# Kernel tuning notes

Measured on AMD Instinct MI355X. Metric: run time of the kernel, lower is better.

## Reference

```python
import jax, jax.numpy as jnp
import numpy as np

B, S, D, H = 1, 512, 128, 128
EPS = 1e-5


def layernorm(x, g, b):
    mu = jnp.mean(x, axis=-1, keepdims=True)
    var = jnp.mean(jnp.square(x - mu), axis=-1, keepdims=True)
    return (x - mu) * jax.lax.rsqrt(var + EPS) * g + b


def setup_inputs() -> dict:
    key = jax.random.key(0)
    ks = jax.random.split(key, 10)
    scale_d = 1.0 / np.sqrt(D)
    scale_h = 1.0 / np.sqrt(H)
    return {
        "x": jax.random.normal(ks[0], (B, S, S, D), dtype=jnp.float32),
        "mask": jax.random.uniform(ks[1], (B, S, S), dtype=jnp.float32),
        "norm_g": jnp.ones((D,), jnp.float32),
        "norm_b": jnp.zeros((D,), jnp.float32),
        "Wl": jax.random.normal(ks[2], (H, D), jnp.float32) * scale_d,
        "Wr": jax.random.normal(ks[3], (H, D), jnp.float32) * scale_d,
        "Wlg": jax.random.normal(ks[4], (H, D), jnp.float32) * scale_d,
        "Wrg": jax.random.normal(ks[5], (H, D), jnp.float32) * scale_d,
        "Wog": jax.random.normal(ks[6], (H, D), jnp.float32) * scale_d,
        "out_norm_g": jnp.ones((H,), jnp.float32),
        "out_norm_b": jnp.zeros((H,), jnp.float32),
        "Wout": jax.random.normal(ks[7], (D, H), jnp.float32) * scale_h,
    }


def reference(x, mask, norm_g, norm_b, Wl, Wr, Wlg, Wrg, Wog, out_norm_g, out_norm_b, Wout):
    # x: [B,S,S,D], mask: [B,S,S]
    xn = layernorm(x, norm_g, norm_b)
    m = mask[..., None]  # [B,S,S,1]
    left = (xn @ Wl.T) * m * jax.nn.sigmoid(xn @ Wlg.T)   # [B,S,S,H]
    right = (xn @ Wr.T) * m * jax.nn.sigmoid(xn @ Wrg.T)  # [B,S,S,H]
    out_gate = jax.nn.sigmoid(xn @ Wog.T)                  # [B,S,S,H]
    # per-channel triangular contraction over k
    out = jnp.einsum('bikd,bjkd->bijd', left, right)       # [B,S,S,H]
    out = layernorm(out, out_norm_g, out_norm_b) * out_gate
    return out @ Wout.T  # [B,S,S,D]
```

## Files before the change

### kernel.cpp

```cpp
#include <hip/hip_runtime.h>
#include <hip/hip_bf16.h>
#include <cstdint>

typedef unsigned short u16;
typedef unsigned int   u32;
typedef __bf16 bf16x8 __attribute__((ext_vector_type(8)));
typedef float  f32x4  __attribute__((ext_vector_type(4)));

#define S_    512
#define D_    128
#define H_    128
#define NPOS_ (S_ * S_)
#define LN_EPS 1e-5f

__device__ __forceinline__ u16 f2bf(float f) {
  union { __hip_bfloat16 h; u16 u; } cv;
  cv.h = __float2bfloat16(f);
  return cv.u;
}
__device__ __forceinline__ float bflo(u32 p) { return __uint_as_float(p << 16); }
__device__ __forceinline__ float bfhi(u32 p) { return __uint_as_float(p & 0xffff0000u); }
__device__ __forceinline__ float sigmoidf_(float x) { return 1.f / (1.f + __expf(-x)); }

__device__ __forceinline__ void gld16(const void* g, void* l) {
  __builtin_amdgcn_global_load_lds(
      (const __attribute__((address_space(1))) void*)g,
      (__attribute__((address_space(3))) void*)l, 16, 0, 0);
}

template <int CPR, int TOTAL>
__device__ __forceinline__ void stage_tile(const char* gbase, int ld_bytes, char* lds, int tid) {
#pragma unroll
  for (int c = tid; c < TOTAL; c += 256) {
    int row = c / CPR;
    int col = c - row * CPR;
    gld16(gbase + (size_t)row * ld_bytes + (size_t)col * 16, lds + (size_t)c * 16);
  }
}

__global__ __launch_bounds__(256) void k_prep(
    const float* __restrict__ wl, const float* __restrict__ wlg,
    const float* __restrict__ wr, const float* __restrict__ wrg,
    const float* __restrict__ wog, const float* __restrict__ wout,
    u16* __restrict__ wb) {
  int i = blockIdx.x * 256 + threadIdx.x;
  int m = i >> 14, o = i & 16383;
  const float* src = (m == 0) ? wl : (m == 1) ? wlg : (m == 2) ? wr
                   : (m == 3) ? wrg : (m == 4) ? wog : wout;
  wb[i] = f2bf(src[o]);
}

__global__ __launch_bounds__(256) void k_ln(
    const float* __restrict__ x, const float* __restrict__ ng,
    const float* __restrict__ nb, u32* __restrict__ xn) {
  const int l  = threadIdx.x & 63;
  const int wid = (blockIdx.x * 256 + threadIdx.x) >> 6;
  const int nw  = (gridDim.x * 256) >> 6;
  const float2 gg = ((const float2*)ng)[l];
  const float2 bb = ((const float2*)nb)[l];
  for (int row = wid; row < NPOS_; row += nw) {
    float2 v = ((const float2*)(x + (size_t)row * D_))[l];
    float s = v.x + v.y;
    float q = v.x * v.x + v.y * v.y;
#pragma unroll
    for (int off = 32; off >= 1; off >>= 1) {
      s += __shfl_xor(s, off);
      q += __shfl_xor(q, off);
    }
    float mu  = s * (1.f / 128.f);
    float var = q * (1.f / 128.f) - mu * mu;
    float rs  = rsqrtf(var + LN_EPS);
    float a = (v.x - mu) * rs * gg.x + bb.x;
    float b = (v.y - mu) * rs * gg.y + bb.y;
    xn[(size_t)row * 64 + l] = (u32)f2bf(a) | ((u32)f2bf(b) << 16);
  }
}

__global__ __launch_bounds__(256, 2) void k_proj(
    const u16* __restrict__ xn, const float* __restrict__ mask,
    const u16* __restrict__ wb, u16* __restrict__ left_t,
    u16* __restrict__ right_t, u16* __restrict__ gate_t) {
  __shared__ u16 Bs[128 * 64];
  __shared__ u16 As0[128 * 64];
  __shared__ u16 As1[128 * 64];
  const int g   = blockIdx.y;
  const int r0  = blockIdx.x * 128;
  const int tid = threadIdx.x;
  const int w = tid >> 6, l = tid & 63;
  const int wr = w >> 1, wc = w & 1;
  const u16* W0 = wb + (size_t)((g == 2) ? 4 : 2 * g) * (H_ * D_);
  const u16* W1 = wb + (size_t)(2 * g + 1) * (H_ * D_);

  const f32x4 vz = {0.f, 0.f, 0.f, 0.f};
  f32x4 acc0[4][4], acc1[4][4];
#pragma unroll
  for (int i = 0; i < 4; ++i)
#pragma unroll
    for (int j = 0; j < 4; ++j) { acc0[i][j] = vz; acc1[i][j] = vz; }

#pragma unroll
  for (int kt = 0; kt < 2; ++kt) {
    stage_tile<8, 1024>((const char*)xn + ((size_t)r0 * D_ + kt * 64) * 2, D_ * 2, (char*)Bs, tid);
    stage_tile<8, 1024>((const char*)W0 + (size_t)(kt * 64) * 2, D_ * 2, (char*)As0, tid);
    if (g < 2)
      stage_tile<8, 1024>((const char*)W1 + (size_t)(kt * 64) * 2, D_ * 2, (char*)As1, tid);
    __syncthreads();
#pragma unroll
    for (int kk = 0; kk < 2; ++kk) {
      const int ko = kk * 32 + (l >> 4) * 8;
      bf16x8 bfr[4], a0[4], a1[4];
#pragma unroll
      for (int ni = 0; ni < 4; ++ni)
        bfr[ni] = *(const bf16x8*)&Bs[(wc * 64 + ni * 16 + (l & 15)) * 64 + ko];
#pragma unroll
      for (int mi = 0; mi < 4; ++mi)
        a0[mi] = *(const bf16x8*)&As0[(wr * 64 + mi * 16 + (l & 15)) * 64 + ko];
      if (g < 2) {
#pragma unroll
        for (int mi = 0; mi < 4; ++mi)
          a1[mi] = *(const bf16x8*)&As1[(wr * 64 + mi * 16 + (l & 15)) * 64 + ko];
      }
#pragma unroll
      for (int mi = 0; mi < 4; ++mi)
#pragma unroll
        for (int ni = 0; ni < 4; ++ni) {
          acc0[mi][ni] = __builtin_amdgcn_mfma_f32_16x16x32_bf16(a0[mi], bfr[ni], acc0[mi][ni], 0, 0, 0);
          if (g < 2)
            acc1[mi][ni] = __builtin_amdgcn_mfma_f32_16x16x32_bf16(a1[mi], bfr[ni], acc1[mi][ni], 0, 0, 0);
        }
    }
    __syncthreads();
  }

  const int quad = l >> 4, lc = l & 15;
  u16* dst = (g == 0) ? left_t : (g == 1) ? right_t : gate_t;
#pragma unroll
  for (int ni = 0; ni < 4; ++ni) {
    const int r = r0 + wc * 64 + ni * 16 + lc;
    const float mk = (g < 2) ? mask[r] : 0.f;
#pragma unroll
    for (int mi = 0; mi < 4; ++mi) {
#pragma unroll
      for (int reg = 0; reg < 4; ++reg) {
        const int hrow = wr * 64 + mi * 16 + quad * 4 + reg;
        float v0 = acc0[mi][ni][reg];
        float o;
        if (g < 2) o = v0 * mk * sigmoidf_(acc1[mi][ni][reg]);
        else       o = sigmoidf_(v0);
        dst[(size_t)hrow * NPOS_ + r] = f2bf(o);
      }
    }
  }
}

__global__ __launch_bounds__(256, 2) void k_einsum(
    const u16* __restrict__ left_t, const u16* __restrict__ right_t,
    u16* __restrict__ out_t) {
  const int d = blockIdx.x;
  const int t = blockIdx.y;
  const int i0 = (t >> 2) * 128, j0 = (t & 3) * 128;
  __shared__ u16 As[128 * 64], Bs[128 * 64];
  const u16* L = left_t + (size_t)d * NPOS_;
  const u16* R = right_t + (size_t)d * NPOS_;
  const int tid = threadIdx.x;
  const int w = tid >> 6, l = tid & 63;
  const int wr = w >> 1, wc = w & 1;

  const f32x4 vz = {0.f, 0.f, 0.f, 0.f};
  f32x4 acc[4][4];
#pragma unroll
  for (int i = 0; i < 4; ++i)
#pragma unroll
    for (int j = 0; j < 4; ++j) acc[i][j] = vz;

  for (int kt = 0; kt < 8; ++kt) {
    stage_tile<8, 1024>((const char*)L + ((size_t)i0 * S_ + kt * 64) * 2, S_ * 2, (char*)As, tid);
    stage_tile<8, 1024>((const char*)R + ((size_t)j0 * S_ + kt * 64) * 2, S_ * 2, (char*)Bs, tid);
    __syncthreads();
#pragma unroll
    for (int kk = 0; kk < 2; ++kk) {
      const int ko = kk * 32 + (l >> 4) * 8;
      bf16x8 a[4], b[4];
#pragma unroll
      for (int mi = 0; mi < 4; ++mi)
        a[mi] = *(const bf16x8*)&As[(wr * 64 + mi * 16 + (l & 15)) * 64 + ko];
#pragma unroll
      for (int ni = 0; ni < 4; ++ni)
        b[ni] = *(const bf16x8*)&Bs[(wc * 64 + ni * 16 + (l & 15)) * 64 + ko];
#pragma unroll
      for (int mi = 0; mi < 4; ++mi)
#pragma unroll
        for (int ni = 0; ni < 4; ++ni)
          acc[mi][ni] = __builtin_amdgcn_mfma_f32_16x16x32_bf16(a[mi], b[ni], acc[mi][ni], 0, 0, 0);
    }
    __syncthreads();
  }

  const int quad = l >> 4, lc = l & 15;
  u16* O = out_t + (size_t)d * NPOS_;
#pragma unroll
  for (int mi = 0; mi < 4; ++mi)
#pragma unroll
    for (int ni = 0; ni < 4; ++ni) {
      const int col = j0 + wc * 64 + ni * 16 + lc;
#pragma unroll
      for (int reg = 0; reg < 4; ++reg) {
        const int row = i0 + wr * 64 + mi * 16 + quad * 4 + reg;
        O[(size_t)row * S_ + col] = f2bf(acc[mi][ni][reg]);
      }
    }
}

__global__ __launch_bounds__(256, 2) void k_final(
    const u16* __restrict__ out_t, const u16* __restrict__ gate_t,
    const float* __restrict__ og, const float* __restrict__ ob,
    const u16* __restrict__ wout_b, float* __restrict__ out) {
  __shared__ u16 A_lds[128 * 136];
  __shared__ u16 Wlds[128 * 128];
  __shared__ float psum[4][128], pq[4][128];
  __shared__ float mu_s[128], rs_s[128];
  const int tid = threadIdx.x, w = tid >> 6, l = tid & 63;
  const int r0 = blockIdx.x * 128;

  stage_tile<16, 2048>((const char*)wout_b, 256, (char*)Wlds, tid);

  float s0 = 0.f, s1 = 0.f, q0 = 0.f, q1 = 0.f;
  for (int it = 0; it < 32; ++it) {
    int d = it * 4 + w;
    u32 p = *(const u32*)&out_t[(size_t)d * NPOS_ + r0 + 2 * l];
    float f0 = bflo(p), f1 = bfhi(p);
    s0 += f0; s1 += f1; q0 += f0 * f0; q1 += f1 * f1;
  }
  psum[w][2 * l] = s0; psum[w][2 * l + 1] = s1;
  pq[w][2 * l] = q0;   pq[w][2 * l + 1] = q1;
  __syncthreads();
  if (tid < 128) {
    float s = psum[0][tid] + psum[1][tid] + psum[2][tid] + psum[3][tid];
    float q = pq[0][tid] + pq[1][tid] + pq[2][tid] + pq[3][tid];
    float mu  = s * (1.f / 128.f);
    float var = q * (1.f / 128.f) - mu * mu;
    mu_s[tid] = mu;
    rs_s[tid] = rsqrtf(var + LN_EPS);
  }
  __syncthreads();

  for (int it = 0; it < 32; ++it) {
    int d = it * 4 + w;
    u32 p  = *(const u32*)&out_t[(size_t)d * NPOS_ + r0 + 2 * l];
    u32 gp = *(const u32*)&gate_t[(size_t)d * NPOS_ + r0 + 2 * l];
    float gd = og[d], bd = ob[d];
    float f0 = bflo(p), f1 = bfhi(p);
    float g0 = bflo(gp), g1 = bfhi(gp);
    int ja = 2 * l, jb = 2 * l + 1;
    float a0 = ((f0 - mu_s[ja]) * rs_s[ja] * gd + bd) * g0;
    float a1 = ((f1 - mu_s[jb]) * rs_s[jb] * gd + bd) * g1;
    A_lds[(size_t)ja * 136 + d] = f2bf(a0);
    A_lds[(size_t)jb * 136 + d] = f2bf(a1);
  }
  __syncthreads();

  const int wr = w >> 1, wc = w & 1;
  const f32x4 vz = {0.f, 0.f, 0.f, 0.f};
  f32x4 acc[4][4];
#pragma unroll
  for (int i = 0; i < 4; ++i)
#pragma unroll
    for (int j = 0; j < 4; ++j) acc[i][j] = vz;
#pragma unroll
  for (int kk = 0; kk < 4; ++kk) {
    const int ko = kk * 32 + (l >> 4) * 8;
    bf16x8 a[4], b[4];
#pragma unroll
    for (int mi = 0; mi < 4; ++mi)
      a[mi] = *(const bf16x8*)&A_lds[(wr * 64 + mi * 16 + (l & 15)) * 136 + ko];
#pragma unroll
    for (int ni = 0; ni < 4; ++ni)
      b[ni] = *(const bf16x8*)&Wlds[(wc * 64 + ni * 16 + (l & 15)) * 128 + ko];
#pragma unroll
    for (int mi = 0; mi < 4; ++mi)
#pragma unroll
      for (int ni = 0; ni < 4; ++ni)
        acc[mi][ni] = __builtin_amdgcn_mfma_f32_16x16x32_bf16(a[mi], b[ni], acc[mi][ni], 0, 0, 0);
  }
  const int quad = l >> 4, lc = l & 15;
#pragma unroll
  for (int mi = 0; mi < 4; ++mi)
#pragma unroll
    for (int ni = 0; ni < 4; ++ni) {
      const int dout = wc * 64 + ni * 16 + lc;
#pragma unroll
      for (int reg = 0; reg < 4; ++reg) {
        const int row = r0 + wr * 64 + mi * 16 + quad * 4 + reg;
        out[(size_t)row * D_ + dout] = acc[mi][ni][reg];
      }
    }
}

extern "C" void kernel_launch(void* const* d_in, const int* in_sizes, int n_in,
                              void* d_out, int out_size, void* d_ws, size_t ws_size,
                              hipStream_t stream) {
  const float* x    = (const float*)d_in[0];
  const float* mask = (const float*)d_in[1];
  const float* ng   = (const float*)d_in[2];
  const float* nb   = (const float*)d_in[3];
  const float* Wl   = (const float*)d_in[4];
  const float* Wr   = (const float*)d_in[5];
  const float* Wlg  = (const float*)d_in[6];
  const float* Wrg  = (const float*)d_in[7];
  const float* Wog  = (const float*)d_in[8];
  const float* og   = (const float*)d_in[9];
  const float* ob   = (const float*)d_in[10];
  const float* Wout = (const float*)d_in[11];
  float* out = (float*)d_out;

  const size_t SLAB = (size_t)NPOS_ * H_ * 2;
  char* ws = (char*)d_ws;
  u16* xn      = (u16*)(ws);
  u16* left_t  = (u16*)(ws + SLAB);
  u16* right_t = (u16*)(ws + 2 * SLAB);
  u16* gate_t  = (u16*)(ws + 3 * SLAB);
  u16* wb      = (u16*)(ws + 4 * SLAB);
  u16* out_t   = xn;
  if (ws_size < 4 * SLAB + 6 * H_ * D_ * sizeof(u16)) return;

  k_prep<<<384, 256, 0, stream>>>(Wl, Wlg, Wr, Wrg, Wog, Wout, wb);
  k_ln<<<2048, 256, 0, stream>>>(x, ng, nb, (u32*)xn);
  k_proj<<<dim3(2048, 3), 256, 0, stream>>>(xn, mask, wb, left_t, right_t, gate_t);
  k_einsum<<<dim3(128, 16), 256, 0, stream>>>(left_t, right_t, out_t);
  k_final<<<2048, 256, 0, stream>>>(out_t, gate_t, og, ob, wb + 5 * H_ * D_, out);
}
```

Baseline: 495.1 us.

## Swizzle LDS tiles, split projection into pair and gate kernels, raise occupancy

Adds an XOR swizzle to every global-to-LDS staging path and fragment read to remove LDS bank conflicts in the MFMA GEMMs. The projection kernel is split into a 512-thread pair kernel, where value and gate waves each own one accumulator set and exchange sigmoids through LDS, and a separate gate-only kernel, so no block carries a second unused accumulator set. Launch bounds are raised to 4 blocks per CU. The bf16 conversion is replaced by manual round-to-nearest-even bit math and sigmoid uses a hardware reciprocal. This adds an extra LDS round trip and barrier in the pair kernel and one more kernel launch.

```diff
diff --git a/kernel.cpp b/kernel.cpp
--- a/kernel.cpp
+++ b/kernel.cpp
@@ -14,13 +14,21 @@
 #define LN_EPS 1e-5f
 
 __device__ __forceinline__ u16 f2bf(float f) {
-  union { __hip_bfloat16 h; u16 u; } cv;
-  cv.h = __float2bfloat16(f);
-  return cv.u;
+  u32 u = __float_as_uint(f);
+  u += 0x7fff + ((u >> 16) & 1);
+  return (u16)(u >> 16);
+}
+__device__ __forceinline__ u32 f2bf2(float lo, float hi) {
+  u32 a = __float_as_uint(lo); a += 0x7fff + ((a >> 16) & 1);
+  u32 b = __float_as_uint(hi); b += 0x7fff + ((b >> 16) & 1);
+  return (a >> 16) | (b & 0xffff0000u);
 }
 __device__ __forceinline__ float bflo(u32 p) { return __uint_as_float(p << 16); }
 __device__ __forceinline__ float bfhi(u32 p) { return __uint_as_float(p & 0xffff0000u); }
-__device__ __forceinline__ float sigmoidf_(float x) { return 1.f / (1.f + __expf(-x)); }
+__device__ __forceinline__ float bf2f(u16 v) { return __uint_as_float((u32)v << 16); }
+__device__ __forceinline__ float sigmoidf_(float x) {
+  return __builtin_amdgcn_rcpf(1.f + __expf(-x));
+}
 
 __device__ __forceinline__ void gld16(const void* g, void* l) {
   __builtin_amdgcn_global_load_lds(
@@ -28,14 +36,23 @@
       (__attribute__((address_space(3))) void*)l, 16, 0, 0);
 }
 
-template <int CPR, int TOTAL>
-__device__ __forceinline__ void stage_tile(const char* gbase, int ld_bytes, char* lds, int tid) {
-#pragma unroll
-  for (int c = tid; c < TOTAL; c += 256) {
-    int row = c / CPR;
-    int col = c - row * CPR;
-    gld16(gbase + (size_t)row * ld_bytes + (size_t)col * 16, lds + (size_t)c * 16);
-  }
+template <int CPR, int TOTAL, int THREADS>
+__device__ __forceinline__ void stage_sw(const char* gbase, int ld_bytes, char* lds, int tid) {
+#pragma unroll
+  for (int c = tid; c < TOTAL; c += THREADS) {
+    int row  = c / CPR;
+    int colL = c & (CPR - 1);
+    int colG = colL ^ (row & (CPR - 1));
+    gld16(gbase + (size_t)row * ld_bytes + (size_t)colG * 16, lds + (size_t)c * 16);
+  }
+}
+__device__ __forceinline__ bf16x8 frag8(const u16* lds, int row, int ko) {
+  int chunk = (ko >> 3) ^ (row & 7);
+  return *(const bf16x8*)&lds[row * 64 + (chunk << 3)];
+}
+__device__ __forceinline__ bf16x8 frag16(const u16* lds, int row, int ko) {
+  int chunk = (ko >> 3) ^ (row & 15);
+  return *(const bf16x8*)&lds[row * 128 + (chunk << 3)];
 }
 
 __global__ __launch_bounds__(256) void k_prep(
@@ -72,88 +89,147 @@
     float rs  = rsqrtf(var + LN_EPS);
     float a = (v.x - mu) * rs * gg.x + bb.x;
     float b = (v.y - mu) * rs * gg.y + bb.y;
-    xn[(size_t)row * 64 + l] = (u32)f2bf(a) | ((u32)f2bf(b) << 16);
-  }
-}
-
-__global__ __launch_bounds__(256, 2) void k_proj(
+    xn[(size_t)row * 64 + l] = f2bf2(a, b);
+  }
+}
+
+__global__ __launch_bounds__(512, 4) void k_proj_pair(
     const u16* __restrict__ xn, const float* __restrict__ mask,
     const u16* __restrict__ wb, u16* __restrict__ left_t,
-    u16* __restrict__ right_t, u16* __restrict__ gate_t) {
+    u16* __restrict__ right_t) {
   __shared__ u16 Bs[128 * 64];
-  __shared__ u16 As0[128 * 64];
-  __shared__ u16 As1[128 * 64];
+  __shared__ u16 As[2 * 128 * 64];
   const int g   = blockIdx.y;
   const int r0  = blockIdx.x * 128;
   const int tid = threadIdx.x;
   const int w = tid >> 6, l = tid & 63;
-  const int wr = w >> 1, wc = w & 1;
-  const u16* W0 = wb + (size_t)((g == 2) ? 4 : 2 * g) * (H_ * D_);
-  const u16* W1 = wb + (size_t)(2 * g + 1) * (H_ * D_);
+  const int role = w >> 2, sub = w & 3;
+  const int wr = sub >> 1, wc = sub & 1;
+  const u16* Wv = wb + (size_t)(2 * g) * (H_ * D_);
+  const u16* Wg = Wv + H_ * D_;
+  const u16* Amine = As + role * (128 * 64);
 
   const f32x4 vz = {0.f, 0.f, 0.f, 0.f};
-  f32x4 acc0[4][4], acc1[4][4];
+  f32x4 acc[4][4];
 #pragma unroll
   for (int i = 0; i < 4; ++i)
 #pragma unroll
-    for (int j = 0; j < 4; ++j) { acc0[i][j] = vz; acc1[i][j] = vz; }
+    for (int j = 0; j < 4; ++j) acc[i][j] = vz;
 
 #pragma unroll
   for (int kt = 0; kt < 2; ++kt) {
-    stage_tile<8, 1024>((const char*)xn + ((size_t)r0 * D_ + kt * 64) * 2, D_ * 2, (char*)Bs, tid);
-    stage_tile<8, 1024>((const char*)W0 + (size_t)(kt * 64) * 2, D_ * 2, (char*)As0, tid);
-    if (g < 2)
-      stage_tile<8, 1024>((const char*)W1 + (size_t)(kt * 64) * 2, D_ * 2, (char*)As1, tid);
+    stage_sw<8, 1024, 512>((const char*)xn + ((size_t)r0 * D_ + kt * 64) * 2, D_ * 2, (char*)Bs, tid);
+    stage_sw<8, 1024, 512>((const char*)Wv + (size_t)(kt * 64) * 2, D_ * 2, (char*)As, tid);
+    stage_sw<8, 1024, 512>((const char*)Wg + (size_t)(kt * 64) * 2, D_ * 2, (char*)(As + 128 * 64), tid);
     __syncthreads();
 #pragma unroll
     for (int kk = 0; kk < 2; ++kk) {
       const int ko = kk * 32 + (l >> 4) * 8;
-      bf16x8 bfr[4], a0[4], a1[4];
-#pragma unroll
-      for (int ni = 0; ni < 4; ++ni)
-        bfr[ni] = *(const bf16x8*)&Bs[(wc * 64 + ni * 16 + (l & 15)) * 64 + ko];
-#pragma unroll
-      for (int mi = 0; mi < 4; ++mi)
-        a0[mi] = *(const bf16x8*)&As0[(wr * 64 + mi * 16 + (l & 15)) * 64 + ko];
-      if (g < 2) {
-#pragma unroll
-        for (int mi = 0; mi < 4; ++mi)
-          a1[mi] = *(const bf16x8*)&As1[(wr * 64 + mi * 16 + (l & 15)) * 64 + ko];
+      bf16x8 bfr[4];
+#pragma unroll
+      for (int ni = 0; ni < 4; ++ni)
+        bfr[ni] = frag8(Bs, wc * 64 + ni * 16 + (l & 15), ko);
+#pragma unroll
+      for (int mi = 0; mi < 4; ++mi) {
+        bf16x8 a = frag8(Amine, wr * 64 + mi * 16 + (l & 15), ko);
+#pragma unroll
+        for (int ni = 0; ni < 4; ++ni)
+          acc[mi][ni] = __builtin_amdgcn_mfma_f32_16x16x32_bf16(a, bfr[ni], acc[mi][ni], 0, 0, 0);
       }
-#pragma unroll
-      for (int mi = 0; mi < 4; ++mi)
-#pragma unroll
-        for (int ni = 0; ni < 4; ++ni) {
-          acc0[mi][ni] = __builtin_amdgcn_mfma_f32_16x16x32_bf16(a0[mi], bfr[ni], acc0[mi][ni], 0, 0, 0);
-          if (g < 2)
-            acc1[mi][ni] = __builtin_amdgcn_mfma_f32_16x16x32_bf16(a1[mi], bfr[ni], acc1[mi][ni], 0, 0, 0);
+    }
+    __syncthreads();
+  }
+
+  const int quad = l >> 4, lc = l & 15;
+  u16* G = As;
+  if (role == 1) {
+#pragma unroll
+    for (int mi = 0; mi < 4; ++mi)
+#pragma unroll
+      for (int ni = 0; ni < 4; ++ni)
+#pragma unroll
+        for (int reg = 0; reg < 4; ++reg) {
+          int idx = (mi * 4 + ni) * 4 + reg;
+          G[(sub * 64 + idx) * 64 + l] = f2bf(sigmoidf_(acc[mi][ni][reg]));
         }
+  }
+  __syncthreads();
+  if (role == 0) {
+    u16* dst = (g == 0) ? left_t : right_t;
+    float mk[4];
+#pragma unroll
+    for (int ni = 0; ni < 4; ++ni) mk[ni] = mask[r0 + wc * 64 + ni * 16 + lc];
+#pragma unroll
+    for (int mi = 0; mi < 4; ++mi)
+#pragma unroll
+      for (int ni = 0; ni < 4; ++ni)
+#pragma unroll
+        for (int reg = 0; reg < 4; ++reg) {
+          int idx = (mi * 4 + ni) * 4 + reg;
+          float sg = bf2f(G[(sub * 64 + idx) * 64 + l]);
+          int r = r0 + wc * 64 + ni * 16 + lc;
+          int hrow = wr * 64 + mi * 16 + quad * 4 + reg;
+          dst[(size_t)hrow * NPOS_ + r] = f2bf(acc[mi][ni][reg] * mk[ni] * sg);
+        }
+  }
+}
+
+__global__ __launch_bounds__(256, 4) void k_proj_gate(
+    const u16* __restrict__ xn, const u16* __restrict__ wb,
+    u16* __restrict__ gate_t) {
+  __shared__ u16 Bs[128 * 64];
+  __shared__ u16 As0[128 * 64];
+  const int r0  = blockIdx.x * 128;
+  const int tid = threadIdx.x;
+  const int w = tid >> 6, l = tid & 63;
+  const int wr = w >> 1, wc = w & 1;
+  const u16* W0 = wb + (size_t)4 * (H_ * D_);
+
+  const f32x4 vz = {0.f, 0.f, 0.f, 0.f};
+  f32x4 acc[4][4];
+#pragma unroll
+  for (int i = 0; i < 4; ++i)
+#pragma unroll
+    for (int j = 0; j < 4; ++j) acc[i][j] = vz;
+
+#pragma unroll
+  for (int kt = 0; kt < 2; ++kt) {
+    stage_sw<8, 1024, 256>((const char*)xn + ((size_t)r0 * D_ + kt * 64) * 2, D_ * 2, (char*)Bs, tid);
+    stage_sw<8, 1024, 256>((const char*)W0 + (size_t)(kt * 64) * 2, D_ * 2, (char*)As0, tid);
+    __syncthreads();
+#pragma unroll
+    for (int kk = 0; kk < 2; ++kk) {
+      const int ko = kk * 32 + (l >> 4) * 8;
+      bf16x8 bfr[4];
+#pragma unroll
+      for (int ni = 0; ni < 4; ++ni)
+        bfr[ni] = frag8(Bs, wc * 64 + ni * 16 + (l & 15), ko);
+#pragma unroll
+      for (int mi = 0; mi < 4; ++mi) {
+        bf16x8 a = frag8(As0, wr * 64 + mi * 16 + (l & 15), ko);
+#pragma unroll
+        for (int ni = 0; ni < 4; ++ni)
+          acc[mi][ni] = __builtin_amdgcn_mfma_f32_16x16x32_bf16(a, bfr[ni], acc[mi][ni], 0, 0, 0);
+      }
     }
     __syncthreads();
   }
 
   const int quad = l >> 4, lc = l & 15;
-  u16* dst = (g == 0) ? left_t : (g == 1) ? right_t : gate_t;
 #pragma unroll
   for (int ni = 0; ni < 4; ++ni) {
     const int r = r0 + wc * 64 + ni * 16 + lc;
-    const float mk = (g < 2) ? mask[r] : 0.f;
-#pragma unroll
-    for (int mi = 0; mi < 4; ++mi) {
+#pragma unroll
+    for (int mi = 0; mi < 4; ++mi)
 #pragma unroll
       for (int reg = 0; reg < 4; ++reg) {
         const int hrow = wr * 64 + mi * 16 + quad * 4 + reg;
-        float v0 = acc0[mi][ni][reg];
-        float o;
-        if (g < 2) o = v0 * mk * sigmoidf_(acc1[mi][ni][reg]);
-        else       o = sigmoidf_(v0);
-        dst[(size_t)hrow * NPOS_ + r] = f2bf(o);
+        gate_t[(size_t)hrow * NPOS_ + r] = f2bf(sigmoidf_(acc[mi][ni][reg]));
       }
-    }
-  }
-}
-
-__global__ __launch_bounds__(256, 2) void k_einsum(
+  }
+}
+
+__global__ __launch_bounds__(256, 4) void k_einsum(
     const u16* __restrict__ left_t, const u16* __restrict__ right_t,
     u16* __restrict__ out_t) {
   const int d = blockIdx.x;
@@ -174,8 +250,8 @@
     for (int j = 0; j < 4; ++j) acc[i][j] = vz;
 
   for (int kt = 0; kt < 8; ++kt) {
-    stage_tile<8, 1024>((const char*)L + ((size_t)i0 * S_ + kt * 64) * 2, S_ * 2, (char*)As, tid);
-    stage_tile<8, 1024>((const char*)R + ((size_t)j0 * S_ + kt * 64) * 2, S_ * 2, (char*)Bs, tid);
+    stage_sw<8, 1024, 256>((const char*)L + ((size_t)i0 * S_ + kt * 64) * 2, S_ * 2, (char*)As, tid);
+    stage_sw<8, 1024, 256>((const char*)R + ((size_t)j0 * S_ + kt * 64) * 2, S_ * 2, (char*)Bs, tid);
     __syncthreads();
 #pragma unroll
     for (int kk = 0; kk < 2; ++kk) {
@@ -183,10 +259,10 @@
       bf16x8 a[4], b[4];
 #pragma unroll
       for (int mi = 0; mi < 4; ++mi)
-        a[mi] = *(const bf16x8*)&As[(wr * 64 + mi * 16 + (l & 15)) * 64 + ko];
-#pragma unroll
-      for (int ni = 0; ni < 4; ++ni)
-        b[ni] = *(const bf16x8*)&Bs[(wc * 64 + ni * 16 + (l & 15)) * 64 + ko];
+        a[mi] = frag8(As, wr * 64 + mi * 16 + (l & 15), ko);
+#pragma unroll
+      for (int ni = 0; ni < 4; ++ni)
+        b[ni] = frag8(Bs, wc * 64 + ni * 16 + (l & 15), ko);
 #pragma unroll
       for (int mi = 0; mi < 4; ++mi)
 #pragma unroll
@@ -222,7 +298,7 @@
   const int tid = threadIdx.x, w = tid >> 6, l = tid & 63;
   const int r0 = blockIdx.x * 128;
 
-  stage_tile<16, 2048>((const char*)wout_b, 256, (char*)Wlds, tid);
+  stage_sw<16, 2048, 256>((const char*)wout_b, 256, (char*)Wlds, tid);
 
   float s0 = 0.f, s1 = 0.f, q0 = 0.f, q1 = 0.f;
   for (int it = 0; it < 32; ++it) {
@@ -252,10 +328,8 @@
     float f0 = bflo(p), f1 = bfhi(p);
     float g0 = bflo(gp), g1 = bfhi(gp);
     int ja = 2 * l, jb = 2 * l + 1;
-    float a0 = ((f0 - mu_s[ja]) * rs_s[ja] * gd + bd) * g0;
-    float a1 = ((f1 - mu_s[jb]) * rs_s[jb] * gd + bd) * g1;
-    A_lds[(size_t)ja * 136 + d] = f2bf(a0);
-    A_lds[(size_t)jb * 136 + d] = f2bf(a1);
+    A_lds[(size_t)ja * 136 + d] = f2bf(((f0 - mu_s[ja]) * rs_s[ja] * gd + bd) * g0);
+    A_lds[(size_t)jb * 136 + d] = f2bf(((f1 - mu_s[jb]) * rs_s[jb] * gd + bd) * g1);
   }
   __syncthreads();
 
@@ -275,7 +349,7 @@
       a[mi] = *(const bf16x8*)&A_lds[(wr * 64 + mi * 16 + (l & 15)) * 136 + ko];
 #pragma unroll
     for (int ni = 0; ni < 4; ++ni)
-      b[ni] = *(const bf16x8*)&Wlds[(wc * 64 + ni * 16 + (l & 15)) * 128 + ko];
+      b[ni] = frag16(Wlds, wc * 64 + ni * 16 + (l & 15), ko);
 #pragma unroll
     for (int mi = 0; mi < 4; ++mi)
 #pragma unroll
@@ -325,7 +399,8 @@
 
   k_prep<<<384, 256, 0, stream>>>(Wl, Wlg, Wr, Wrg, Wog, Wout, wb);
   k_ln<<<2048, 256, 0, stream>>>(x, ng, nb, (u32*)xn);
-  k_proj<<<dim3(2048, 3), 256, 0, stream>>>(xn, mask, wb, left_t, right_t, gate_t);
+  k_proj_pair<<<dim3(2048, 2), 512, 0, stream>>>(xn, mask, wb, left_t, right_t);
+  k_proj_gate<<<2048, 256, 0, stream>>>(xn, wb, gate_t);
   k_einsum<<<dim3(128, 16), 256, 0, stream>>>(left_t, right_t, out_t);
   k_final<<<2048, 256, 0, stream>>>(out_t, gate_t, og, ob, wb + 5 * H_ * D_, out);
 }
```

After: 610.6 us. 1.23x slower.
